# Kernel tuning notes

Hardware: AMD Instinct MI355X
Metric: run time of the kernel (lower is better)

Reference implementation:

```python
import jax, jax.numpy as jnp
import numpy as np

PROTO_DIM = 512
PROTO_NUM = 4096
BSZ = 256
SUBTEXT_NUM = 64
TEMP = 0.9


def setup_inputs() -> dict:
    key = jax.random.key(0)
    k1, k2, k3 = jax.random.split(key, 3)
    subtexts = jax.random.normal(k1, (BSZ, SUBTEXT_NUM, PROTO_DIM), dtype=jnp.float32)
    prototype = jax.random.normal(k2, (PROTO_NUM, PROTO_DIM), dtype=jnp.float32)
    uniform = jax.random.uniform(k3, (BSZ * SUBTEXT_NUM, PROTO_NUM), dtype=jnp.float32)
    return {"subtexts": subtexts, "prototype": prototype, "uniform": uniform}


def reference(subtexts, prototype, uniform):
    # flatten: [N, D] with N = bsz * subtext_num
    flatten = subtexts.reshape(-1, PROTO_DIM)
    # dist: [N, proto_num] = flatten @ prototype.T
    dist = jnp.einsum("nd,pd->np", flatten, prototype)
    # Gumbel noise g = -log(-log(u)), matching torch F.gumbel_softmax sampling
    tiny = jnp.float32(1e-10)
    gumbel = -jnp.log(-jnp.log(uniform + tiny) + tiny)
    # noisy logits -> softmax over codebook dim (tau = curr_temp)
    soft_one_hot = jax.nn.softmax((dist + gumbel) / jnp.float32(TEMP), axis=1)
    # output: [N, D] soft codebook lookup
    output = jnp.einsum("np,pd->nd", soft_one_hot, prototype)
    proto_idx = jnp.argmax(soft_one_hot, axis=1)
    proto_loss = jnp.mean(jnp.abs(output - flatten))
    return (output, proto_loss, proto_idx)
```

## Files before the change

### kernel.cpp

```cpp
#include <hip/hip_runtime.h>
#include <math.h>

#define NROWS 16384
#define DIM   512
#define NPROTO 4096
#define TINV (1.0f / 0.9f)
#define LOSS_OFF ((size_t)NROWS * DIM)
#define IDX_OFF  ((size_t)NROWS * DIM + 1)
#define LCAP 128
#define LTHR 10.0f

typedef __attribute__((ext_vector_type(4))) int i32x4;
typedef __attribute__((ext_vector_type(4))) float f32x4;

__global__ void zero_loss_kernel(float* out) { out[LOSS_OFF] = 0.0f; }

static __device__ __forceinline__ void gl_lds16(const void* g, void* l) {
    __builtin_amdgcn_global_load_lds((const __attribute__((address_space(1))) unsigned int*)g,
                                     (__attribute__((address_space(3))) unsigned int*)l, 16, 0, 0);
}

__global__ __launch_bounds__(256)
void split_i8_kernel(const float* __restrict__ src, char* __restrict__ d1, char* __restrict__ d0,
                     float* __restrict__ dScale, int nrows)
{
    __shared__ __align__(16) char s1[32][512];
    __shared__ __align__(16) char s0[32][512];
    const int tid = threadIdx.x;
    const int row = tid >> 3;
    const int sub = tid & 7;
    const int r0 = blockIdx.x * 32;
    const float* rp = &src[(size_t)(r0 + row) * DIM + sub * 64];
    float v[64];
    float mx = 1e-20f;
#pragma unroll
    for (int i = 0; i < 16; ++i) {
        float4 f = *(const float4*)&rp[i * 4];
        v[i*4+0] = f.x; v[i*4+1] = f.y; v[i*4+2] = f.z; v[i*4+3] = f.w;
        mx = fmaxf(mx, fmaxf(fmaxf(fabsf(f.x), fabsf(f.y)), fmaxf(fabsf(f.z), fabsf(f.w))));
    }
#pragma unroll
    for (int off = 1; off < 8; off <<= 1) mx = fmaxf(mx, __shfl_xor(mx, off));
    const float s   = mx * (1.0f / 16256.0f);
    const float inv = 16256.0f / mx;
    if (sub == 0) dScale[r0 + row] = s;
#pragma unroll
    for (int i = 0; i < 64; ++i) {
        float q  = v[i] * inv;
        float a1 = rintf(q * (1.0f / 128.0f));
        float a0 = rintf(q - 128.0f * a1);
        s1[row][sub * 64 + i] = (char)(int)a1;
        s0[row][sub * 64 + i] = (char)(int)a0;
    }
    __syncthreads();
#pragma unroll
    for (int i = 0; i < 4; ++i) {
        int idx = i * 256 + tid;
        int g = idx >> 5;
        int rr = idx & 31;
        size_t o = ((size_t)g * nrows + r0 + rr) * 16;
        *(ulonglong2*)&d1[o] = *(const ulonglong2*)&s1[rr][g * 16];
        *(ulonglong2*)&d0[o] = *(const ulonglong2*)&s0[rr][g * 16];
    }
}

#define BM 32
#define BN 256
#define NCHUNK (NPROTO / BN)
#define NT 8

__global__ __launch_bounds__(256, 2)
void attr_proto_i8(const float* __restrict__ A, const float* __restrict__ Pr,
                   const float* __restrict__ U, float* __restrict__ out,
                   uint2* __restrict__ gList,
                   const char* __restrict__ wsA1, const char* __restrict__ wsA0,
                   const char* __restrict__ wsP1, const char* __restrict__ wsP0,
                   const float* __restrict__ wsSA, const float* __restrict__ wsSP)
{
    __shared__ __align__(16) char sA[2][2][4][BM][16];
    __shared__ __align__(16) char sP[2][2][4][BN][16];
    __shared__ float wMax[4][BM];
    __shared__ float mRun[BM];
    __shared__ float smSA[BM];
    __shared__ int cnt[BM];

    const int tid = threadIdx.x;
    const int w = tid >> 6;
    const int lane = tid & 63;
    const int l4 = lane & 15;
    const int lh = lane >> 4;
    const int row0 = blockIdx.x * BM;

    if (tid < BM) { mRun[tid] = -1e30f; cnt[tid] = 0; smSA[tid] = wsSA[row0 + tid]; }

    const char* gp[9];
    int str9[9], fx9[9], bstr9[9];
    char* ld9[9];
#pragma unroll
    for (int si = 0; si < 9; ++si) {
        int s = w * 9 + si;
        if (s < 4) {
            int limb = s >> 1, gpair = s & 1;
            int g = gpair * 2 + (lane >> 5);
            gp[si]  = (limb ? wsA0 : wsA1) + ((size_t)g * NROWS + row0 + (lane & 31)) * 16;
            str9[si] = 4 * NROWS * 16;
            fx9[si]  = -NT * 4 * NROWS * 16;
            ld9[si]  = &sA[0][limb][gpair * 2][0][0] + (size_t)lane * 16;
            bstr9[si] = 2 * 4 * BM * 16;
        } else {
            int p = s - 4;
            int limb = p >> 4, rem = p & 15, g = rem >> 2, q = rem & 3;
            gp[si]  = (limb ? wsP0 : wsP1) + ((size_t)g * NPROTO + q * 64 + lane) * 16;
            str9[si] = 4 * NPROTO * 16;
            fx9[si]  = -NT * 4 * NPROTO * 16 + BN * 16;
            ld9[si]  = &sP[0][limb][g][q * 64][0] + (size_t)lane * 16;
            bstr9[si] = 2 * 4 * BN * 16;
        }
    }
#define DO_STAGE(b) { _Pragma("unroll") for (int si = 0; si < 9; ++si) { \
        gl_lds16(gp[si], ld9[si] + ((b) ? bstr9[si] : 0)); gp[si] += str9[si]; } }
#define DO_FIXUP() { _Pragma("unroll") for (int si = 0; si < 9; ++si) gp[si] += fx9[si]; }

    i32x4 c11[2][4], c10[2][4], c01[2][4];
    auto COMPUTE = [&](int cur) {
        i32x4 a1[2], a0[2], b1[4], b0[4];
#pragma unroll
        for (int mf = 0; mf < 2; ++mf) {
            a1[mf] = *(const i32x4*)&sA[cur][0][lh][mf * 16 + l4][0];
            a0[mf] = *(const i32x4*)&sA[cur][1][lh][mf * 16 + l4][0];
        }
#pragma unroll
        for (int nf = 0; nf < 4; ++nf) {
            b1[nf] = *(const i32x4*)&sP[cur][0][lh][w * 64 + nf * 16 + l4][0];
            b0[nf] = *(const i32x4*)&sP[cur][1][lh][w * 64 + nf * 16 + l4][0];
        }
#pragma unroll
        for (int mf = 0; mf < 2; ++mf)
#pragma unroll
            for (int nf = 0; nf < 4; ++nf) {
                c11[mf][nf] = __builtin_amdgcn_mfma_i32_16x16x64_i8(a1[mf], b1[nf], c11[mf][nf], 0, 0, 0);
                c10[mf][nf] = __builtin_amdgcn_mfma_i32_16x16x64_i8(a1[mf], b0[nf], c10[mf][nf], 0, 0, 0);
                c01[mf][nf] = __builtin_amdgcn_mfma_i32_16x16x64_i8(a0[mf], b1[nf], c01[mf][nf], 0, 0, 0);
            }
    };

    DO_STAGE(0);
    __syncthreads();

    for (int ch = 0; ch < NCHUNK; ++ch) {
        const int pbase = ch * BN;
        float spv[4];
#pragma unroll
        for (int nf = 0; nf < 4; ++nf) spv[nf] = wsSP[pbase + w * 64 + nf * 16 + l4];
#pragma unroll
        for (int mf = 0; mf < 2; ++mf)
#pragma unroll
            for (int nf = 0; nf < 4; ++nf) {
                c11[mf][nf] = i32x4{0,0,0,0}; c10[mf][nf] = i32x4{0,0,0,0}; c01[mf][nf] = i32x4{0,0,0,0};
            }

#pragma unroll 2
        for (int t = 0; t < NT; ++t) {
            const int cur = t & 1;
            if (t < NT - 1) {
                DO_STAGE(cur ^ 1);
            } else if (ch + 1 < NCHUNK) {
                DO_FIXUP(); DO_STAGE(cur ^ 1);
            }
            COMPUTE(cur);
            __syncthreads();
        }

        f32x4 zf[2][4];
#pragma unroll
        for (int mf = 0; mf < 2; ++mf) {
            const int rb = row0 + mf * 16 + lh * 4;
#pragma unroll
            for (int nf = 0; nf < 4; ++nf)
#pragma unroll
                for (int r = 0; r < 4; ++r) {
                    float dist = smSA[mf * 16 + lh * 4 + r] * spv[nf] *
                                 (16384.0f * (float)c11[mf][nf][r] +
                                  128.0f * ((float)c10[mf][nf][r] + (float)c01[mf][nf][r]));
                    float u = U[(size_t)(rb + r) * NPROTO + pbase + w * 64 + nf * 16 + l4];
                    float g = -__logf(-__logf(u + 1e-10f) + 1e-10f);
                    zf[mf][nf][r] = (dist + g) * TINV;
                }
        }
#pragma unroll
        for (int mf = 0; mf < 2; ++mf) {
            f32x4 rm;
#pragma unroll
            for (int r = 0; r < 4; ++r)
                rm[r] = fmaxf(fmaxf(zf[mf][0][r], zf[mf][1][r]), fmaxf(zf[mf][2][r], zf[mf][3][r]));
#pragma unroll
            for (int off = 1; off < 16; off <<= 1)
#pragma unroll
                for (int r = 0; r < 4; ++r) rm[r] = fmaxf(rm[r], __shfl_xor(rm[r], off));
#pragma unroll
            for (int r = 0; r < 4; ++r) {
                const int rl = mf * 16 + lh * 4 + r;
                float thrv = fmaxf(mRun[rl], rm[r]) - LTHR;
#pragma unroll
                for (int nf = 0; nf < 4; ++nf) {
                    float z = zf[mf][nf][r];
                    if (z > thrv) {
                        int pos = atomicAdd(&cnt[rl], 1);
                        if (pos < LCAP) {
                            uint2 en; en.x = __float_as_uint(z); en.y = (unsigned)(pbase + w * 64 + nf * 16 + l4);
                            gList[(size_t)(row0 + rl) * LCAP + pos] = en;
                        }
                    }
                }
            }
            if (l4 == 0)
#pragma unroll
                for (int r = 0; r < 4; ++r) wMax[w][mf * 16 + lh * 4 + r] = rm[r];
        }
        __syncthreads();
        if (tid < BM) {
            float gm = fmaxf(fmaxf(wMax[0][tid], wMax[1][tid]), fmaxf(wMax[2][tid], wMax[3][tid]));
            mRun[tid] = fmaxf(mRun[tid], gm);
        }
        __syncthreads();
    }
#undef DO_STAGE
#undef DO_FIXUP

    __syncthreads();
    float lossTot = 0.f;
    for (int r = w; r < BM; r += 4) {
        const int row = row0 + r;
        const int c = min(cnt[r], LCAP);
        const uint2* lst = &gList[(size_t)row * LCAP];

        float M = -1e30f;
        for (int e = lane; e < c; e += 64) M = fmaxf(M, __uint_as_float(lst[e].x));
#pragma unroll
        for (int off = 1; off < 64; off <<= 1) M = fmaxf(M, __shfl_xor(M, off));
        const float cutoff = M - LTHR;

        float L = 0.f, bz = -1e30f; int bi = 1 << 30;
        for (int e = lane; e < c; e += 64) {
            float z = __uint_as_float(lst[e].x); int p = (int)lst[e].y;
            if (z > cutoff) {
                L += __expf(z - M);
                if (z > bz || (z == bz && p < bi)) { bz = z; bi = p; }
            }
        }
#pragma unroll
        for (int off = 1; off < 64; off <<= 1) {
            L += __shfl_xor(L, off);
            float oz = __shfl_xor(bz, off); int oi = __shfl_xor(bi, off);
            if (oz > bz || (oz == bz && oi < bi)) { bz = oz; bi = oi; }
        }

        float bestz = -1e30f; int bestp = 1 << 30;
        const float* ap = &A[(size_t)row * DIM];
        for (int e = lane; e < c; e += 64) {
            float z = __uint_as_float(lst[e].x);
            if (z > bz - 3.0f) {
                int p = (int)lst[e].y;
                const float* pp = &Pr[(size_t)p * DIM];
                float d = 0.f;
                for (int k = 0; k < DIM; k += 4) {
                    float4 av = *(const float4*)&ap[k];
                    float4 pv = *(const float4*)&pp[k];
                    d = fmaf(av.x, pv.x, d);
                    d = fmaf(av.y, pv.y, d);
                    d = fmaf(av.z, pv.z, d);
                    d = fmaf(av.w, pv.w, d);
                }
                float u = U[(size_t)row * NPROTO + p];
                float g = -logf(-logf(u + 1e-10f) + 1e-10f);
                float zz = (d + g) * (1.0f / 0.9f);
                if (zz > bestz || (zz == bestz && p < bestp)) { bestz = zz; bestp = p; }
            }
        }
#pragma unroll
        for (int off = 1; off < 64; off <<= 1) {
            float oz = __shfl_xor(bestz, off); int oi = __shfl_xor(bestp, off);
            if (oz > bestz || (oz == bestz && oi < bestp)) { bestz = oz; bestp = oi; }
        }
        if (lane == 0) out[IDX_OFF + row] = (float)bestp;

        float o[8];
#pragma unroll
        for (int q = 0; q < 8; ++q) o[q] = 0.f;
        const float Li = 1.0f / L;
        for (int e = 0; e < c; ++e) {
            uint2 en = lst[e];
            float z = __uint_as_float(en.x);
            if (z > cutoff) {
                float wgt = __expf(z - M) * Li;
                const float* pp = &Pr[(size_t)en.y * DIM + lane * 8];
                float4 p0 = *(const float4*)pp;
                float4 p1 = *(const float4*)(pp + 4);
                o[0] += wgt * p0.x; o[1] += wgt * p0.y; o[2] += wgt * p0.z; o[3] += wgt * p0.w;
                o[4] += wgt * p1.x; o[5] += wgt * p1.y; o[6] += wgt * p1.z; o[7] += wgt * p1.w;
            }
        }
        const float* fr = &A[(size_t)row * DIM + lane * 8];
        float4 f0 = *(const float4*)fr; float4 f1 = *(const float4*)(fr + 4);
        *(float4*)&out[(size_t)row * DIM + lane * 8]     = make_float4(o[0], o[1], o[2], o[3]);
        *(float4*)&out[(size_t)row * DIM + lane * 8 + 4] = make_float4(o[4], o[5], o[6], o[7]);
        lossTot += fabsf(o[0]-f0.x) + fabsf(o[1]-f0.y) + fabsf(o[2]-f0.z) + fabsf(o[3]-f0.w)
                 + fabsf(o[4]-f1.x) + fabsf(o[5]-f1.y) + fabsf(o[6]-f1.z) + fabsf(o[7]-f1.w);
    }
#pragma unroll
    for (int off = 1; off < 64; off <<= 1) lossTot += __shfl_xor(lossTot, off);
    if (lane == 0) atomicAdd(&out[LOSS_OFF], lossTot * (1.0f / ((float)NROWS * (float)DIM)));
}

#define FCAP 192
#define FTHR 20.0f

__global__ __launch_bounds__(256, 1)
void attr_proto_fused_valu(const float* __restrict__ A, const float* __restrict__ Pr,
                           const float* __restrict__ U, float* __restrict__ out)
{
    __shared__ __align__(16) float As[64][64 + 4];
    __shared__ __align__(16) float Bs[128][64 + 4];
    __shared__ float hZ[64][FCAP];
    __shared__ unsigned short hI[64][FCAP];
    __shared__ int cnt[64];
    __shared__ float mArr[64];
    __shared__ float lArr[64];
    __shared__ int pruneFlag;

    const int tid = threadIdx.x;
    const int tx = tid & 31;
    const int ty = tid >> 5;
    const int row0 = blockIdx.x * 64;

    for (int r = tid; r < 64; r += 256) cnt[r] = 0;
    if (tid == 0) pruneFlag = 0;

    float m[8], l[8], bz[8];
    int bi[8];
#pragma unroll
    for (int i = 0; i < 8; ++i) { m[i] = -INFINITY; l[i] = 0.0f; bz[i] = -INFINITY; bi[i] = 0; }
    __syncthreads();

    for (int ch = 0; ch < 32; ++ch) {
        const int pbase = ch * 128;
        float acc[8][4];
#pragma unroll
        for (int i = 0; i < 8; ++i)
#pragma unroll
            for (int j = 0; j < 4; ++j) acc[i][j] = 0.0f;

        for (int kk = 0; kk < DIM; kk += 64) {
#pragma unroll
            for (int q = 0; q < 4; ++q) {
                int lin = tid + q * 256;
                int lr = lin >> 4; int kq = (lin & 15) << 2;
                *(float4*)&As[lr][kq] = *(const float4*)&A[(size_t)(row0 + lr) * DIM + kk + kq];
            }
#pragma unroll
            for (int q = 0; q < 8; ++q) {
                int lin = tid + q * 256;
                int pr = lin >> 4; int kq = (lin & 15) << 2;
                *(float4*)&Bs[pr][kq] = *(const float4*)&Pr[(size_t)(pbase + pr) * DIM + kk + kq];
            }
            __syncthreads();
#pragma unroll 4
            for (int k4 = 0; k4 < 64; k4 += 4) {
                float4 av[8], bv[4];
#pragma unroll
                for (int i = 0; i < 8; ++i) av[i] = *(const float4*)&As[ty * 8 + i][k4];
#pragma unroll
                for (int j = 0; j < 4; ++j) bv[j] = *(const float4*)&Bs[tx + 32 * j][k4];
#pragma unroll
                for (int i = 0; i < 8; ++i)
#pragma unroll
                    for (int j = 0; j < 4; ++j) {
                        acc[i][j] += av[i].x * bv[j].x; acc[i][j] += av[i].y * bv[j].y;
                        acc[i][j] += av[i].z * bv[j].z; acc[i][j] += av[i].w * bv[j].w;
                    }
            }
            __syncthreads();
        }
#pragma unroll
        for (int i = 0; i < 8; ++i) {
            const int ri = ty * 8 + i;
            const size_t urow = (size_t)(row0 + ri) * NPROTO + pbase;
            float z[4]; float lmax = -INFINITY;
#pragma unroll
            for (int j = 0; j < 4; ++j) {
                float u = U[urow + tx + 32 * j];
                float g = -logf(-logf(u + 1e-10f) + 1e-10f);
                z[j] = (acc[i][j] + g) * TINV;
                lmax = fmaxf(lmax, z[j]);
            }
#pragma unroll
            for (int off = 16; off; off >>= 1) lmax = fmaxf(lmax, __shfl_xor(lmax, off, 32));
            const float mn = fmaxf(m[i], lmax);
            float s = 0.0f;
#pragma unroll
            for (int j = 0; j < 4; ++j) s += expf(z[j] - mn);
#pragma unroll
            for (int off = 16; off; off >>= 1) s += __shfl_xor(s, off, 32);
            l[i] = l[i] * expf(m[i] - mn) + s;
            m[i] = mn;
#pragma unroll
            for (int j = 0; j < 4; ++j) {
                const int p = pbase + tx + 32 * j;
                if (z[j] > bz[i]) { bz[i] = z[j]; bi[i] = p; }
                if (z[j] > mn - FTHR) {
                    int pos = atomicAdd(&cnt[ri], 1);
                    if (pos < FCAP) { hZ[ri][pos] = z[j]; hI[ri][pos] = (unsigned short)p; }
                }
            }
            if (tx == 0) {
                mArr[ri] = mn;
                if (cnt[ri] > 64) atomicOr(&pruneFlag, 1);
            }
        }
        __syncthreads();
        if (pruneFlag) {
            for (int r = 0; r < 64; ++r) {
                const int c0 = min(cnt[r], FCAP);
                if (c0 > 64) {
                    const float thr = mArr[r] - FTHR;
                    float ez = 0.0f; int ei = 0; bool keep = false;
                    if (tid < c0) { ez = hZ[r][tid]; ei = hI[r][tid]; keep = (ez > thr); }
                    __syncthreads();
                    if (tid == 0) cnt[r] = 0;
                    __syncthreads();
                    if (keep) { int pos = atomicAdd(&cnt[r], 1); hZ[r][pos] = ez; hI[r][pos] = (unsigned short)ei; }
                    __syncthreads();
                }
            }
            if (tid == 0) pruneFlag = 0;
            __syncthreads();
        }
    }
#pragma unroll
    for (int i = 0; i < 8; ++i) {
        const int ri = ty * 8 + i;
        float vz = bz[i]; int vi = bi[i];
#pragma unroll
        for (int off = 16; off; off >>= 1) {
            float oz = __shfl_xor(vz, off, 32); int oi = __shfl_xor(vi, off, 32);
            if (oz > vz || (oz == vz && oi < vi)) { vz = oz; vi = oi; }
        }
        if (tx == 0) { lArr[ri] = l[i]; out[IDX_OFF + row0 + ri] = (float)vi; }
    }
    __syncthreads();

    const int wv = tid >> 6;
    const int lane = tid & 63;
    float lossAcc = 0.0f;
    for (int r = wv; r < 64; r += 4) {
        const int grow = row0 + r;
        const int c = min(cnt[r], FCAP);
        const float mm = mArr[r];
        const float li = 1.0f / lArr[r];
        float o[8];
#pragma unroll
        for (int q = 0; q < 8; ++q) o[q] = 0.0f;
        for (int e = 0; e < c; ++e) {
            const float wg = expf(hZ[r][e] - mm) * li;
            const float* pp = &Pr[(size_t)hI[r][e] * DIM + lane * 8];
            float4 p0 = *(const float4*)pp; float4 p1 = *(const float4*)(pp + 4);
            o[0] += wg * p0.x; o[1] += wg * p0.y; o[2] += wg * p0.z; o[3] += wg * p0.w;
            o[4] += wg * p1.x; o[5] += wg * p1.y; o[6] += wg * p1.z; o[7] += wg * p1.w;
        }
        const float* fr = &A[(size_t)grow * DIM + lane * 8];
        float4 f0 = *(const float4*)fr; float4 f1 = *(const float4*)(fr + 4);
        *(float4*)&out[(size_t)grow * DIM + lane * 8]     = make_float4(o[0], o[1], o[2], o[3]);
        *(float4*)&out[(size_t)grow * DIM + lane * 8 + 4] = make_float4(o[4], o[5], o[6], o[7]);
        lossAcc += fabsf(o[0]-f0.x) + fabsf(o[1]-f0.y) + fabsf(o[2]-f0.z) + fabsf(o[3]-f0.w)
                 + fabsf(o[4]-f1.x) + fabsf(o[5]-f1.y) + fabsf(o[6]-f1.z) + fabsf(o[7]-f1.w);
    }
#pragma unroll
    for (int off = 32; off; off >>= 1) lossAcc += __shfl_xor(lossAcc, off, 64);
    if (lane == 0) atomicAdd(&out[LOSS_OFF], lossAcc * (1.0f / ((float)NROWS * (float)DIM)));
}

extern "C" void kernel_launch(void* const* d_in, const int* in_sizes, int n_in,
                              void* d_out, int out_size, void* d_ws, size_t ws_size,
                              hipStream_t stream)
{
    const float* A  = (const float*)d_in[0];
    const float* Pr = (const float*)d_in[1];
    const float* U  = (const float*)d_in[2];
    float* out = (float*)d_out;

    const size_t szA = (size_t)NROWS * DIM;
    const size_t szP = (size_t)NPROTO * DIM;
    const size_t scABytes = (size_t)NROWS * sizeof(float);
    const size_t scPBytes = (size_t)NPROTO * sizeof(float);
    const size_t listBytes = (size_t)NROWS * LCAP * sizeof(uint2);
    const size_t need = 2 * szA + 2 * szP + scABytes + scPBytes + listBytes;

    zero_loss_kernel<<<1, 1, 0, stream>>>(out);

    if (ws_size >= need) {
        char*  wsA1 = (char*)d_ws;
        char*  wsA0 = wsA1 + szA;
        char*  wsP1 = wsA0 + szA;
        char*  wsP0 = wsP1 + szP;
        float* wsSA = (float*)(wsP0 + szP);
        float* wsSP = wsSA + NROWS;
        uint2* gList = (uint2*)((char*)(wsSP + NPROTO));
        split_i8_kernel<<<NROWS / 32, 256, 0, stream>>>(A, wsA1, wsA0, wsSA, NROWS);
        split_i8_kernel<<<NPROTO / 32, 256, 0, stream>>>(Pr, wsP1, wsP0, wsSP, NPROTO);
        attr_proto_i8<<<NROWS / BM, 256, 0, stream>>>(A, Pr, U, out, gList,
                                                      wsA1, wsA0, wsP1, wsP0, wsSA, wsSP);
    } else {
        attr_proto_fused_valu<<<NROWS / 64, 256, 0, stream>>>(A, Pr, U, out);
    }
}
```

Measured before the change: 455.7 us.

## Keep A tile resident in LDS and give each wave private prototype staging without barriers

The A int8 limbs for the 32-row block are loaded into LDS once, and each wave stages only its own 64 prototypes into a private LDS region. This removes the block-wide __syncthreads in the K loop and the cross-wave running-max exchange; the running max is now tracked per wave. The split kernel now writes 32-byte groups instead of 16-byte ones. In exchange, each wave waits synchronously on vmcnt(0) with no double buffering, so load latency is exposed. Thresholding uses a per-wave max, so more candidates pass, and LCAP is raised to 160 to make room.

```diff
diff --git a/kernel.cpp b/kernel.cpp
--- a/kernel.cpp
+++ b/kernel.cpp
@@ -7,11 +7,10 @@
 #define TINV (1.0f / 0.9f)
 #define LOSS_OFF ((size_t)NROWS * DIM)
 #define IDX_OFF  ((size_t)NROWS * DIM + 1)
-#define LCAP 128
+#define LCAP 160
 #define LTHR 10.0f
 
 typedef __attribute__((ext_vector_type(4))) int i32x4;
-typedef __attribute__((ext_vector_type(4))) float f32x4;
 
 __global__ void zero_loss_kernel(float* out) { out[LOSS_OFF] = 0.0f; }
 
@@ -19,6 +18,8 @@
     __builtin_amdgcn_global_load_lds((const __attribute__((address_space(1))) unsigned int*)g,
                                      (__attribute__((address_space(3))) unsigned int*)l, 16, 0, 0);
 }
+#define WAIT_VM0() asm volatile("s_waitcnt vmcnt(0)" ::: "memory")
+#define SBAR() __builtin_amdgcn_sched_barrier(0)
 
 __global__ __launch_bounds__(256)
 void split_i8_kernel(const float* __restrict__ src, char* __restrict__ d1, char* __restrict__ d0,
@@ -54,13 +55,15 @@
     }
     __syncthreads();
 #pragma unroll
-    for (int i = 0; i < 4; ++i) {
+    for (int i = 0; i < 2; ++i) {
         int idx = i * 256 + tid;
         int g = idx >> 5;
         int rr = idx & 31;
-        size_t o = ((size_t)g * nrows + r0 + rr) * 16;
-        *(ulonglong2*)&d1[o] = *(const ulonglong2*)&s1[rr][g * 16];
-        *(ulonglong2*)&d0[o] = *(const ulonglong2*)&s0[rr][g * 16];
+        size_t o = ((size_t)g * nrows + r0 + rr) * 32;
+        *(ulonglong2*)&d1[o]      = *(const ulonglong2*)&s1[rr][g * 32];
+        *(ulonglong2*)&d1[o + 16] = *(const ulonglong2*)&s1[rr][g * 32 + 16];
+        *(ulonglong2*)&d0[o]      = *(const ulonglong2*)&s0[rr][g * 32];
+        *(ulonglong2*)&d0[o + 16] = *(const ulonglong2*)&s0[rr][g * 32 + 16];
     }
 }
 
@@ -70,18 +73,15 @@
 #define NT 8
 
 __global__ __launch_bounds__(256, 2)
-void attr_proto_i8(const float* __restrict__ A, const float* __restrict__ Pr,
-                   const float* __restrict__ U, float* __restrict__ out,
-                   uint2* __restrict__ gList,
-                   const char* __restrict__ wsA1, const char* __restrict__ wsA0,
-                   const char* __restrict__ wsP1, const char* __restrict__ wsP0,
-                   const float* __restrict__ wsSA, const float* __restrict__ wsSP)
+void attr_proto_wa2(const float* __restrict__ A, const float* __restrict__ Pr,
+                    const float* __restrict__ U, float* __restrict__ out,
+                    uint2* __restrict__ gList,
+                    const char* __restrict__ wsA1, const char* __restrict__ wsA0,
+                    const char* __restrict__ wsP1, const char* __restrict__ wsP0,
+                    const float* __restrict__ wsSA, const float* __restrict__ wsSP)
 {
-    __shared__ __align__(16) char sA[2][2][4][BM][16];
-    __shared__ __align__(16) char sP[2][2][4][BN][16];
-    __shared__ float wMax[4][BM];
-    __shared__ float mRun[BM];
-    __shared__ float smSA[BM];
+    __shared__ __align__(16) char aL[2][16][32][32];
+    __shared__ __align__(16) char pL[4][2][2][64][32];
     __shared__ int cnt[BM];
 
     const int tid = threadIdx.x;
@@ -91,61 +91,59 @@
     const int lh = lane >> 4;
     const int row0 = blockIdx.x * BM;
 
-    if (tid < BM) { mRun[tid] = -1e30f; cnt[tid] = 0; smSA[tid] = wsSA[row0 + tid]; }
-
-    const char* gp[9];
-    int str9[9], fx9[9], bstr9[9];
-    char* ld9[9];
-#pragma unroll
-    for (int si = 0; si < 9; ++si) {
-        int s = w * 9 + si;
-        if (s < 4) {
-            int limb = s >> 1, gpair = s & 1;
-            int g = gpair * 2 + (lane >> 5);
-            gp[si]  = (limb ? wsA0 : wsA1) + ((size_t)g * NROWS + row0 + (lane & 31)) * 16;
-            str9[si] = 4 * NROWS * 16;
-            fx9[si]  = -NT * 4 * NROWS * 16;
-            ld9[si]  = &sA[0][limb][gpair * 2][0][0] + (size_t)lane * 16;
-            bstr9[si] = 2 * 4 * BM * 16;
-        } else {
-            int p = s - 4;
-            int limb = p >> 4, rem = p & 15, g = rem >> 2, q = rem & 3;
-            gp[si]  = (limb ? wsP0 : wsP1) + ((size_t)g * NPROTO + q * 64 + lane) * 16;
-            str9[si] = 4 * NPROTO * 16;
-            fx9[si]  = -NT * 4 * NPROTO * 16 + BN * 16;
-            ld9[si]  = &sP[0][limb][g][q * 64][0] + (size_t)lane * 16;
-            bstr9[si] = 2 * 4 * BN * 16;
-        }
-    }
-#define DO_STAGE(b) { _Pragma("unroll") for (int si = 0; si < 9; ++si) { \
-        gl_lds16(gp[si], ld9[si] + ((b) ? bstr9[si] : 0)); gp[si] += str9[si]; } }
-#define DO_FIXUP() { _Pragma("unroll") for (int si = 0; si < 9; ++si) gp[si] += fx9[si]; }
+    if (tid < BM) cnt[tid] = 0;
+
+    const char* gpP[8];
+    char* ldP[8];
+#pragma unroll
+    for (int si = 0; si < 8; ++si) {
+        int limb = si >> 2, g2l = (si >> 1) & 1, half = si & 1;
+        gpP[si] = (limb ? wsP0 : wsP1)
+                + ((size_t)g2l * NPROTO + w * 64 + half * 32 + (lane >> 1)) * 32 + (lane & 1) * 16;
+        ldP[si] = &pL[w][limb][g2l][half * 32][0] + (size_t)lane * 16;
+    }
+    const int strP = 2 * NPROTO * 32;
+    const int fxP  = -16 * NPROTO * 32 + BN * 32;
+#define STAGE_P() { _Pragma("unroll") for (int si = 0; si < 8; ++si) { \
+        gl_lds16(gpP[si], ldP[si]); gpP[si] += strP; } }
+#define FIXUP_P() { _Pragma("unroll") for (int si = 0; si < 8; ++si) gpP[si] += fxP; }
+
+#pragma unroll
+    for (int q = 0; q < 8; ++q) {
+        int s = w * 8 + q;
+        int limb = s >> 4, g2 = s & 15;
+        const char* base = limb ? wsA0 : wsA1;
+        gl_lds16(base + ((size_t)g2 * NROWS + row0 + (lane >> 1)) * 32 + (lane & 1) * 16,
+                 &aL[limb][g2][0][0] + (size_t)lane * 16);
+    }
+    __syncthreads();
+
+    float sav[8], mloc[8];
+#pragma unroll
+    for (int mf = 0; mf < 2; ++mf)
+#pragma unroll
+        for (int r = 0; r < 4; ++r) {
+            sav[mf * 4 + r]  = wsSA[row0 + mf * 16 + lh * 4 + r];
+            mloc[mf * 4 + r] = -1e30f;
+        }
 
     i32x4 c11[2][4], c10[2][4], c01[2][4];
-    auto COMPUTE = [&](int cur) {
-        i32x4 a1[2], a0[2], b1[4], b0[4];
-#pragma unroll
-        for (int mf = 0; mf < 2; ++mf) {
-            a1[mf] = *(const i32x4*)&sA[cur][0][lh][mf * 16 + l4][0];
-            a0[mf] = *(const i32x4*)&sA[cur][1][lh][mf * 16 + l4][0];
-        }
-#pragma unroll
-        for (int nf = 0; nf < 4; ++nf) {
-            b1[nf] = *(const i32x4*)&sP[cur][0][lh][w * 64 + nf * 16 + l4][0];
-            b0[nf] = *(const i32x4*)&sP[cur][1][lh][w * 64 + nf * 16 + l4][0];
-        }
-#pragma unroll
-        for (int mf = 0; mf < 2; ++mf)
-#pragma unroll
-            for (int nf = 0; nf < 4; ++nf) {
-                c11[mf][nf] = __builtin_amdgcn_mfma_i32_16x16x64_i8(a1[mf], b1[nf], c11[mf][nf], 0, 0, 0);
-                c10[mf][nf] = __builtin_amdgcn_mfma_i32_16x16x64_i8(a1[mf], b0[nf], c10[mf][nf], 0, 0, 0);
-                c01[mf][nf] = __builtin_amdgcn_mfma_i32_16x16x64_i8(a0[mf], b1[nf], c01[mf][nf], 0, 0, 0);
-            }
-    };
-
-    DO_STAGE(0);
-    __syncthreads();
+
+#define COMPUTE(T) { \
+    const int g2a = (T) * 2 + (lh >> 1); \
+    const int gsub = (lh & 1) * 16; \
+    i32x4 a1[2], a0[2], b1[4], b0[4]; \
+    _Pragma("unroll") for (int mf = 0; mf < 2; ++mf) { \
+        a1[mf] = *(const i32x4*)&aL[0][g2a][mf * 16 + l4][gsub]; \
+        a0[mf] = *(const i32x4*)&aL[1][g2a][mf * 16 + l4][gsub]; } \
+    _Pragma("unroll") for (int nf = 0; nf < 4; ++nf) { \
+        b1[nf] = *(const i32x4*)&pL[w][0][lh >> 1][nf * 16 + l4][gsub]; \
+        b0[nf] = *(const i32x4*)&pL[w][1][lh >> 1][nf * 16 + l4][gsub]; } \
+    _Pragma("unroll") for (int mf = 0; mf < 2; ++mf) \
+    _Pragma("unroll") for (int nf = 0; nf < 4; ++nf) { \
+        c11[mf][nf] = __builtin_amdgcn_mfma_i32_16x16x64_i8(a1[mf], b1[nf], c11[mf][nf], 0, 0, 0); \
+        c10[mf][nf] = __builtin_amdgcn_mfma_i32_16x16x64_i8(a1[mf], b0[nf], c10[mf][nf], 0, 0, 0); \
+        c01[mf][nf] = __builtin_amdgcn_mfma_i32_16x16x64_i8(a0[mf], b1[nf], c01[mf][nf], 0, 0, 0); } }
 
     for (int ch = 0; ch < NCHUNK; ++ch) {
         const int pbase = ch * BN;
@@ -159,40 +157,34 @@
                 c11[mf][nf] = i32x4{0,0,0,0}; c10[mf][nf] = i32x4{0,0,0,0}; c01[mf][nf] = i32x4{0,0,0,0};
             }
 
-#pragma unroll 2
         for (int t = 0; t < NT; ++t) {
-            const int cur = t & 1;
-            if (t < NT - 1) {
-                DO_STAGE(cur ^ 1);
-            } else if (ch + 1 < NCHUNK) {
-                DO_FIXUP(); DO_STAGE(cur ^ 1);
-            }
-            COMPUTE(cur);
-            __syncthreads();
-        }
-
-        f32x4 zf[2][4];
+            SBAR();
+            STAGE_P();
+            WAIT_VM0();
+            SBAR();
+            COMPUTE(t);
+        }
+        FIXUP_P();
+
 #pragma unroll
         for (int mf = 0; mf < 2; ++mf) {
+            float zf[4][4];
             const int rb = row0 + mf * 16 + lh * 4;
 #pragma unroll
             for (int nf = 0; nf < 4; ++nf)
 #pragma unroll
                 for (int r = 0; r < 4; ++r) {
-                    float dist = smSA[mf * 16 + lh * 4 + r] * spv[nf] *
+                    float dist = sav[mf * 4 + r] * spv[nf] *
                                  (16384.0f * (float)c11[mf][nf][r] +
                                   128.0f * ((float)c10[mf][nf][r] + (float)c01[mf][nf][r]));
                     float u = U[(size_t)(rb + r) * NPROTO + pbase + w * 64 + nf * 16 + l4];
                     float g = -__logf(-__logf(u + 1e-10f) + 1e-10f);
-                    zf[mf][nf][r] = (dist + g) * TINV;
+                    zf[nf][r] = (dist + g) * TINV;
                 }
-        }
-#pragma unroll
-        for (int mf = 0; mf < 2; ++mf) {
-            f32x4 rm;
+            float rm[4];
 #pragma unroll
             for (int r = 0; r < 4; ++r)
-                rm[r] = fmaxf(fmaxf(zf[mf][0][r], zf[mf][1][r]), fmaxf(zf[mf][2][r], zf[mf][3][r]));
+                rm[r] = fmaxf(fmaxf(zf[0][r], zf[1][r]), fmaxf(zf[2][r], zf[3][r]));
 #pragma unroll
             for (int off = 1; off < 16; off <<= 1)
 #pragma unroll
@@ -200,32 +192,27 @@
 #pragma unroll
             for (int r = 0; r < 4; ++r) {
                 const int rl = mf * 16 + lh * 4 + r;
-                float thrv = fmaxf(mRun[rl], rm[r]) - LTHR;
+                float mcur = fmaxf(mloc[mf * 4 + r], rm[r]);
+                mloc[mf * 4 + r] = mcur;
+                float thrv = mcur - LTHR;
 #pragma unroll
                 for (int nf = 0; nf < 4; ++nf) {
-                    float z = zf[mf][nf][r];
+                    float z = zf[nf][r];
                     if (z > thrv) {
                         int pos = atomicAdd(&cnt[rl], 1);
                         if (pos < LCAP) {
-                            uint2 en; en.x = __float_as_uint(z); en.y = (unsigned)(pbase + w * 64 + nf * 16 + l4);
+                            uint2 en; en.x = __float_as_uint(z);
+                            en.y = (unsigned)(pbase + w * 64 + nf * 16 + l4);
                             gList[(size_t)(row0 + rl) * LCAP + pos] = en;
                         }
                     }
                 }
             }
-            if (l4 == 0)
-#pragma unroll
-                for (int r = 0; r < 4; ++r) wMax[w][mf * 16 + lh * 4 + r] = rm[r];
-        }
-        __syncthreads();
-        if (tid < BM) {
-            float gm = fmaxf(fmaxf(wMax[0][tid], wMax[1][tid]), fmaxf(wMax[2][tid], wMax[3][tid]));
-            mRun[tid] = fmaxf(mRun[tid], gm);
-        }
-        __syncthreads();
-    }
-#undef DO_STAGE
-#undef DO_FIXUP
+        }
+    }
+#undef STAGE_P
+#undef FIXUP_P
+#undef COMPUTE
 
     __syncthreads();
     float lossTot = 0.f;
@@ -490,10 +477,8 @@
 
     const size_t szA = (size_t)NROWS * DIM;
     const size_t szP = (size_t)NPROTO * DIM;
-    const size_t scABytes = (size_t)NROWS * sizeof(float);
-    const size_t scPBytes = (size_t)NPROTO * sizeof(float);
     const size_t listBytes = (size_t)NROWS * LCAP * sizeof(uint2);
-    const size_t need = 2 * szA + 2 * szP + scABytes + scPBytes + listBytes;
+    const size_t need = 2 * szA + 2 * szP + (NROWS + NPROTO) * sizeof(float) + listBytes;
 
     zero_loss_kernel<<<1, 1, 0, stream>>>(out);
 
@@ -507,8 +492,8 @@
         uint2* gList = (uint2*)((char*)(wsSP + NPROTO));
         split_i8_kernel<<<NROWS / 32, 256, 0, stream>>>(A, wsA1, wsA0, wsSA, NROWS);
         split_i8_kernel<<<NPROTO / 32, 256, 0, stream>>>(Pr, wsP1, wsP0, wsSP, NPROTO);
-        attr_proto_i8<<<NROWS / BM, 256, 0, stream>>>(A, Pr, U, out, gList,
-                                                      wsA1, wsA0, wsP1, wsP0, wsSA, wsSP);
+        attr_proto_wa2<<<NROWS / BM, 256, 0, stream>>>(A, Pr, U, out, gList,
+                                                       wsA1, wsA0, wsP1, wsP0, wsSA, wsSP);
     } else {
         attr_proto_fused_valu<<<NROWS / 64, 256, 0, stream>>>(A, Pr, U, out);
     }
```

Result: slower. 533.1 us (+17.0%).

## Split post-GEMM softmax/lookup into a separate fully parallel finish kernel

Applied to the files above, without the earlier changes.

The int8 GEMM kernel now only collects the candidate lists and writes per-row counts to the workspace. A new finish kernel handles the per-row softmax, argmax refinement, weighted prototype lookup and loss, using one wave per row across NROWS/4 blocks. This is meant to remove the serial tail, where each GEMM block's four waves looped over 32 rows, and to spread the loss atomics over 64 workspace slots that a final kernel then reduces. In exchange it adds two extra launches and a round trip of the lists and counts through global memory.

```diff
diff --git a/kernel.cpp b/kernel.cpp
--- a/kernel.cpp
+++ b/kernel.cpp
@@ -11,9 +11,9 @@
 #define LTHR 10.0f
 
 typedef __attribute__((ext_vector_type(4))) int i32x4;
-typedef __attribute__((ext_vector_type(4))) float f32x4;
 
 __global__ void zero_loss_kernel(float* out) { out[LOSS_OFF] = 0.0f; }
+__global__ void zero_ws_kernel(float* wsLoss) { wsLoss[threadIdx.x] = 0.0f; }
 
 static __device__ __forceinline__ void gl_lds16(const void* g, void* l) {
     __builtin_amdgcn_global_load_lds((const __attribute__((address_space(1))) unsigned int*)g,
@@ -70,9 +70,8 @@
 #define NT 8
 
 __global__ __launch_bounds__(256, 2)
-void attr_proto_i8(const float* __restrict__ A, const float* __restrict__ Pr,
-                   const float* __restrict__ U, float* __restrict__ out,
-                   uint2* __restrict__ gList,
+void gemm_collect2(const float* __restrict__ U,
+                   int* __restrict__ gCnt, uint2* __restrict__ gList,
                    const char* __restrict__ wsA1, const char* __restrict__ wsA0,
                    const char* __restrict__ wsP1, const char* __restrict__ wsP0,
                    const float* __restrict__ wsSA, const float* __restrict__ wsSP)
@@ -171,7 +170,7 @@
             __syncthreads();
         }
 
-        f32x4 zf[2][4];
+        float zf[2][4][4];
 #pragma unroll
         for (int mf = 0; mf < 2; ++mf) {
             const int rb = row0 + mf * 16 + lh * 4;
@@ -189,7 +188,7 @@
         }
 #pragma unroll
         for (int mf = 0; mf < 2; ++mf) {
-            f32x4 rm;
+            float rm[4];
 #pragma unroll
             for (int r = 0; r < 4; ++r)
                 rm[r] = fmaxf(fmaxf(zf[mf][0][r], zf[mf][1][r]), fmaxf(zf[mf][2][r], zf[mf][3][r]));
@@ -207,7 +206,8 @@
                     if (z > thrv) {
                         int pos = atomicAdd(&cnt[rl], 1);
                         if (pos < LCAP) {
-                            uint2 en; en.x = __float_as_uint(z); en.y = (unsigned)(pbase + w * 64 + nf * 16 + l4);
+                            uint2 en; en.x = __float_as_uint(z);
+                            en.y = (unsigned)(pbase + w * 64 + nf * 16 + l4);
                             gList[(size_t)(row0 + rl) * LCAP + pos] = en;
                         }
                     }
@@ -228,88 +228,104 @@
 #undef DO_FIXUP
 
     __syncthreads();
-    float lossTot = 0.f;
-    for (int r = w; r < BM; r += 4) {
-        const int row = row0 + r;
-        const int c = min(cnt[r], LCAP);
-        const uint2* lst = &gList[(size_t)row * LCAP];
-
-        float M = -1e30f;
-        for (int e = lane; e < c; e += 64) M = fmaxf(M, __uint_as_float(lst[e].x));
-#pragma unroll
-        for (int off = 1; off < 64; off <<= 1) M = fmaxf(M, __shfl_xor(M, off));
-        const float cutoff = M - LTHR;
-
-        float L = 0.f, bz = -1e30f; int bi = 1 << 30;
-        for (int e = lane; e < c; e += 64) {
-            float z = __uint_as_float(lst[e].x); int p = (int)lst[e].y;
-            if (z > cutoff) {
-                L += __expf(z - M);
-                if (z > bz || (z == bz && p < bi)) { bz = z; bi = p; }
-            }
-        }
-#pragma unroll
-        for (int off = 1; off < 64; off <<= 1) {
-            L += __shfl_xor(L, off);
-            float oz = __shfl_xor(bz, off); int oi = __shfl_xor(bi, off);
-            if (oz > bz || (oz == bz && oi < bi)) { bz = oz; bi = oi; }
-        }
-
-        float bestz = -1e30f; int bestp = 1 << 30;
-        const float* ap = &A[(size_t)row * DIM];
-        for (int e = lane; e < c; e += 64) {
-            float z = __uint_as_float(lst[e].x);
-            if (z > bz - 3.0f) {
-                int p = (int)lst[e].y;
-                const float* pp = &Pr[(size_t)p * DIM];
-                float d = 0.f;
-                for (int k = 0; k < DIM; k += 4) {
-                    float4 av = *(const float4*)&ap[k];
-                    float4 pv = *(const float4*)&pp[k];
-                    d = fmaf(av.x, pv.x, d);
-                    d = fmaf(av.y, pv.y, d);
-                    d = fmaf(av.z, pv.z, d);
-                    d = fmaf(av.w, pv.w, d);
-                }
-                float u = U[(size_t)row * NPROTO + p];
-                float g = -logf(-logf(u + 1e-10f) + 1e-10f);
-                float zz = (d + g) * (1.0f / 0.9f);
-                if (zz > bestz || (zz == bestz && p < bestp)) { bestz = zz; bestp = p; }
-            }
-        }
-#pragma unroll
-        for (int off = 1; off < 64; off <<= 1) {
-            float oz = __shfl_xor(bestz, off); int oi = __shfl_xor(bestp, off);
-            if (oz > bestz || (oz == bestz && oi < bestp)) { bestz = oz; bestp = oi; }
-        }
-        if (lane == 0) out[IDX_OFF + row] = (float)bestp;
-
-        float o[8];
-#pragma unroll
-        for (int q = 0; q < 8; ++q) o[q] = 0.f;
-        const float Li = 1.0f / L;
-        for (int e = 0; e < c; ++e) {
-            uint2 en = lst[e];
-            float z = __uint_as_float(en.x);
-            if (z > cutoff) {
-                float wgt = __expf(z - M) * Li;
-                const float* pp = &Pr[(size_t)en.y * DIM + lane * 8];
-                float4 p0 = *(const float4*)pp;
-                float4 p1 = *(const float4*)(pp + 4);
-                o[0] += wgt * p0.x; o[1] += wgt * p0.y; o[2] += wgt * p0.z; o[3] += wgt * p0.w;
-                o[4] += wgt * p1.x; o[5] += wgt * p1.y; o[6] += wgt * p1.z; o[7] += wgt * p1.w;
-            }
-        }
-        const float* fr = &A[(size_t)row * DIM + lane * 8];
-        float4 f0 = *(const float4*)fr; float4 f1 = *(const float4*)(fr + 4);
-        *(float4*)&out[(size_t)row * DIM + lane * 8]     = make_float4(o[0], o[1], o[2], o[3]);
-        *(float4*)&out[(size_t)row * DIM + lane * 8 + 4] = make_float4(o[4], o[5], o[6], o[7]);
-        lossTot += fabsf(o[0]-f0.x) + fabsf(o[1]-f0.y) + fabsf(o[2]-f0.z) + fabsf(o[3]-f0.w)
-                 + fabsf(o[4]-f1.x) + fabsf(o[5]-f1.y) + fabsf(o[6]-f1.z) + fabsf(o[7]-f1.w);
-    }
-#pragma unroll
-    for (int off = 1; off < 64; off <<= 1) lossTot += __shfl_xor(lossTot, off);
-    if (lane == 0) atomicAdd(&out[LOSS_OFF], lossTot * (1.0f / ((float)NROWS * (float)DIM)));
+    if (tid < BM) gCnt[row0 + tid] = cnt[tid];
+}
+
+__global__ __launch_bounds__(256)
+void finish_kernel(const float* __restrict__ A, const float* __restrict__ Pr,
+                   const float* __restrict__ U, float* __restrict__ out,
+                   const int* __restrict__ gCnt, const uint2* __restrict__ gList,
+                   float* __restrict__ wsLoss)
+{
+    const int tid = threadIdx.x;
+    const int lane = tid & 63;
+    const int row = blockIdx.x * 4 + (tid >> 6);
+    const int c = min(gCnt[row], LCAP);
+    const uint2* lst = &gList[(size_t)row * LCAP];
+
+    float M = -1e30f;
+    for (int e = lane; e < c; e += 64) M = fmaxf(M, __uint_as_float(lst[e].x));
+#pragma unroll
+    for (int off = 1; off < 64; off <<= 1) M = fmaxf(M, __shfl_xor(M, off));
+    const float cutoff = M - LTHR;
+
+    float L = 0.f, bz = -1e30f; int bi = 1 << 30;
+    for (int e = lane; e < c; e += 64) {
+        float z = __uint_as_float(lst[e].x); int p = (int)lst[e].y;
+        if (z > cutoff) {
+            L += __expf(z - M);
+            if (z > bz || (z == bz && p < bi)) { bz = z; bi = p; }
+        }
+    }
+#pragma unroll
+    for (int off = 1; off < 64; off <<= 1) {
+        L += __shfl_xor(L, off);
+        float oz = __shfl_xor(bz, off); int oi = __shfl_xor(bi, off);
+        if (oz > bz || (oz == bz && oi < bi)) { bz = oz; bi = oi; }
+    }
+
+    float bestz = -1e30f; int bestp = 1 << 30;
+    const float* ap = &A[(size_t)row * DIM];
+    for (int e = lane; e < c; e += 64) {
+        float z = __uint_as_float(lst[e].x);
+        if (z > bz - 3.0f) {
+            int p = (int)lst[e].y;
+            const float* pp = &Pr[(size_t)p * DIM];
+            float d = 0.f;
+            for (int k = 0; k < DIM; k += 4) {
+                float4 av = *(const float4*)&ap[k];
+                float4 pv = *(const float4*)&pp[k];
+                d = fmaf(av.x, pv.x, d);
+                d = fmaf(av.y, pv.y, d);
+                d = fmaf(av.z, pv.z, d);
+                d = fmaf(av.w, pv.w, d);
+            }
+            float u = U[(size_t)row * NPROTO + p];
+            float g = -logf(-logf(u + 1e-10f) + 1e-10f);
+            float zz = (d + g) * (1.0f / 0.9f);
+            if (zz > bestz || (zz == bestz && p < bestp)) { bestz = zz; bestp = p; }
+        }
+    }
+#pragma unroll
+    for (int off = 1; off < 64; off <<= 1) {
+        float oz = __shfl_xor(bestz, off); int oi = __shfl_xor(bestp, off);
+        if (oz > bestz || (oz == bestz && oi < bestp)) { bestz = oz; bestp = oi; }
+    }
+    if (lane == 0) out[IDX_OFF + row] = (float)bestp;
+
+    float o[8];
+#pragma unroll
+    for (int q = 0; q < 8; ++q) o[q] = 0.f;
+    const float Li = 1.0f / L;
+    for (int e = 0; e < c; ++e) {
+        uint2 en = lst[e];
+        float z = __uint_as_float(en.x);
+        if (z > cutoff) {
+            float wgt = __expf(z - M) * Li;
+            const float* pp = &Pr[(size_t)en.y * DIM + lane * 8];
+            float4 p0 = *(const float4*)pp;
+            float4 p1 = *(const float4*)(pp + 4);
+            o[0] += wgt * p0.x; o[1] += wgt * p0.y; o[2] += wgt * p0.z; o[3] += wgt * p0.w;
+            o[4] += wgt * p1.x; o[5] += wgt * p1.y; o[6] += wgt * p1.z; o[7] += wgt * p1.w;
+        }
+    }
+    const float* fr = &A[(size_t)row * DIM + lane * 8];
+    float4 f0 = *(const float4*)fr; float4 f1 = *(const float4*)(fr + 4);
+    *(float4*)&out[(size_t)row * DIM + lane * 8]     = make_float4(o[0], o[1], o[2], o[3]);
+    *(float4*)&out[(size_t)row * DIM + lane * 8 + 4] = make_float4(o[4], o[5], o[6], o[7]);
+    float lossAcc = fabsf(o[0]-f0.x) + fabsf(o[1]-f0.y) + fabsf(o[2]-f0.z) + fabsf(o[3]-f0.w)
+                  + fabsf(o[4]-f1.x) + fabsf(o[5]-f1.y) + fabsf(o[6]-f1.z) + fabsf(o[7]-f1.w);
+#pragma unroll
+    for (int off = 1; off < 64; off <<= 1) lossAcc += __shfl_xor(lossAcc, off);
+    if (lane == 0) atomicAdd(&wsLoss[blockIdx.x & 63], lossAcc * (1.0f / ((float)NROWS * (float)DIM)));
+}
+
+__global__ void loss_final_kernel(const float* __restrict__ wsLoss, float* __restrict__ out)
+{
+    float s = wsLoss[threadIdx.x];
+#pragma unroll
+    for (int off = 1; off < 64; off <<= 1) s += __shfl_xor(s, off);
+    if (threadIdx.x == 0) out[LOSS_OFF] = s;
 }
 
 #define FCAP 192
@@ -490,12 +506,10 @@
 
     const size_t szA = (size_t)NROWS * DIM;
     const size_t szP = (size_t)NPROTO * DIM;
-    const size_t scABytes = (size_t)NROWS * sizeof(float);
-    const size_t scPBytes = (size_t)NPROTO * sizeof(float);
+    const size_t scBytes  = (size_t)(NROWS + NPROTO) * sizeof(float);
     const size_t listBytes = (size_t)NROWS * LCAP * sizeof(uint2);
-    const size_t need = 2 * szA + 2 * szP + scABytes + scPBytes + listBytes;
-
-    zero_loss_kernel<<<1, 1, 0, stream>>>(out);
+    const size_t cntBytes = (size_t)NROWS * sizeof(int);
+    const size_t need = 2 * szA + 2 * szP + scBytes + listBytes + cntBytes + 64 * sizeof(float);
 
     if (ws_size >= need) {
         char*  wsA1 = (char*)d_ws;
@@ -504,12 +518,18 @@
         char*  wsP0 = wsP1 + szP;
         float* wsSA = (float*)(wsP0 + szP);
         float* wsSP = wsSA + NROWS;
-        uint2* gList = (uint2*)((char*)(wsSP + NPROTO));
+        uint2* gList = (uint2*)(wsSP + NPROTO);
+        int*   gCnt  = (int*)((char*)gList + listBytes);
+        float* wsLoss = (float*)((char*)gCnt + cntBytes);
         split_i8_kernel<<<NROWS / 32, 256, 0, stream>>>(A, wsA1, wsA0, wsSA, NROWS);
         split_i8_kernel<<<NPROTO / 32, 256, 0, stream>>>(Pr, wsP1, wsP0, wsSP, NPROTO);
-        attr_proto_i8<<<NROWS / BM, 256, 0, stream>>>(A, Pr, U, out, gList,
+        zero_ws_kernel<<<1, 64, 0, stream>>>(wsLoss);
+        gemm_collect2<<<NROWS / BM, 256, 0, stream>>>(U, gCnt, gList,
                                                       wsA1, wsA0, wsP1, wsP0, wsSA, wsSP);
+        finish_kernel<<<NROWS / 4, 256, 0, stream>>>(A, Pr, U, out, gCnt, gList, wsLoss);
+        loss_final_kernel<<<1, 64, 0, stream>>>(wsLoss, out);
     } else {
+        zero_loss_kernel<<<1, 1, 0, stream>>>(out);
         attr_proto_fused_valu<<<NROWS / 64, 256, 0, stream>>>(A, Pr, U, out);
     }
 }
```

Measured after the change: 415.0 us. 8.9% less time.
